# Kernel tuning notes

Measured on AMD Instinct MI355X. Metric: run time of the kernel, lower is better.

Reference implementation:

```python
import jax, jax.numpy as jnp
import numpy as np

N_HEAD = 16
HEAD_DIM = 64


def setup_inputs() -> dict:
    key = jax.random.key(0)
    k1, k2, k3 = jax.random.split(key, 3)
    B, T, C = 1, 4096, 1024
    x = jax.random.normal(k1, (B, T, C), dtype=jnp.float32)
    w_attn = jax.random.normal(k2, (3 * C, C), dtype=jnp.float32) * (C ** -0.5)
    w_proj = jax.random.normal(k3, (C, C), dtype=jnp.float32) * (C ** -0.5)
    return {"x": x, "w_attn": w_attn, "w_proj": w_proj}


def reference(x, w_attn, w_proj):
    B, T, C = x.shape
    H, D = N_HEAD, HEAD_DIM
    qkv = jnp.einsum('btc,fc->btf', x, w_attn)  # [B,T,3C]
    q, k, v = jnp.split(qkv, 3, axis=-1)
    # [B,H,T,D]
    q = q.reshape(B, T, H, D).transpose(0, 2, 1, 3)
    k = k.reshape(B, T, H, D).transpose(0, 2, 1, 3)
    v = v.reshape(B, T, H, D).transpose(0, 2, 1, 3)
    scale = 1.0 / (D ** 0.5)
    att = jnp.einsum('bhqd,bhkd->bhqk', q, k) * scale  # [B,H,T,T]
    causal = jnp.tril(jnp.ones((T, T), dtype=bool))
    att = jnp.where(causal[None, None], att, -jnp.inf)
    att = jax.nn.softmax(att, axis=-1)
    y = jnp.einsum('bhqk,bhkd->bhqd', att, v)  # [B,H,T,D]
    y = y.transpose(0, 2, 1, 3).reshape(B, T, C)
    return jnp.einsum('btc,oc->bto', y, w_proj)
```

## Files before the change

### kernel.cpp

```cpp
#include <hip/hip_runtime.h>

typedef unsigned short u16;
typedef __bf16 bf16x8 __attribute__((ext_vector_type(8)));
typedef float f32x4 __attribute__((ext_vector_type(4)));

__device__ __forceinline__ u16 f2bf(float f) {
  union { float f; unsigned u; } v; v.f = f;
  return (u16)((v.u + 0x7fffu + ((v.u >> 16) & 1u)) >> 16);
}
__device__ __forceinline__ float bf2f(u16 h) {
  union { unsigned u; float f; } v; v.u = ((unsigned)h) << 16;
  return v.f;
}

__device__ __forceinline__ unsigned pkbf(float lo, float hi) {
  union { float f; unsigned u; } a, b; a.f = lo; b.f = hi;
  return __builtin_amdgcn_perm(b.u + 0x8000u, a.u + 0x8000u, 0x07060302u);
}

__device__ __forceinline__ float fexp2(float x) {
#if __has_builtin(__builtin_amdgcn_exp2f)
  return __builtin_amdgcn_exp2f(x);
#else
  return exp2f(x);
#endif
}

__device__ __forceinline__ void gld16(const u16* g, u16* l) {
  __builtin_amdgcn_global_load_lds(
      (const __attribute__((address_space(1))) void*)g,
      (__attribute__((address_space(3))) void*)l, 16, 0, 0);
}


__global__ __launch_bounds__(256) void cvt3(
    const float* __restrict__ x, const float* __restrict__ wa,
    const float* __restrict__ wp, u16* __restrict__ xb,
    u16* __restrict__ wab, u16* __restrict__ wpb)
{
  int b = blockIdx.x;
  const float* in; u16* out; int i;
  if (b < 2048)      { in = x;  out = xb;  i = b * 256 + threadIdx.x; }
  else if (b < 3584) { in = wa; out = wab; i = (b - 2048) * 256 + threadIdx.x; }
  else               { in = wp; out = wpb; i = (b - 3584) * 256 + threadIdx.x; }
  const float* p = in + (size_t)i * 8;
  float4 a = *(const float4*)p, c = *(const float4*)(p + 4);
  uint4 o;
  o.x = pkbf(a.x, a.y); o.y = pkbf(a.z, a.w);
  o.z = pkbf(c.x, c.y); o.w = pkbf(c.z, c.w);
  *(uint4*)&out[(size_t)i * 8] = o;
}

__global__ __launch_bounds__(256) void combine2(
    const u16* __restrict__ O0, const u16* __restrict__ O1,
    const float* __restrict__ l0, const float* __restrict__ l1,
    u16* __restrict__ y)
{
  int i = blockIdx.x * 256 + threadIdx.x;
  int e0 = i * 8;
  int row = e0 >> 10, h = (e0 & 1023) >> 6;
  float inv = 1.0f / (l0[row * 16 + h] + l1[row * 16 + h]);
  uint4 a = *(const uint4*)&O0[(size_t)e0];
  uint4 b = *(const uint4*)&O1[(size_t)e0];
  unsigned aw[4] = {a.x, a.y, a.z, a.w}, bw[4] = {b.x, b.y, b.z, b.w};
  uint4 o;
  unsigned ow[4];
#pragma unroll
  for (int j = 0; j < 4; ++j) {
    float lo = (bf2f((u16)(aw[j] & 0xffffu)) + bf2f((u16)(bw[j] & 0xffffu))) * inv;
    float hi = (bf2f((u16)(aw[j] >> 16))     + bf2f((u16)(bw[j] >> 16)))     * inv;
    ow[j] = pkbf(lo, hi);
  }
  o.x = ow[0]; o.y = ow[1]; o.z = ow[2]; o.w = ow[3];
  *(uint4*)&y[(size_t)e0] = o;
}

template<bool COUT_F32, bool VSPLIT>
__global__ __launch_bounds__(256, 3) void gemm_lds(
    const u16* __restrict__ A, const u16* __restrict__ B, void* __restrict__ C,
    u16* __restrict__ C2, int M, int N, int K, int ldc)
{
  __shared__ u16 S[9216];
  u16* As = S;
  u16* Bs = S + 4096;
  const int tid  = threadIdx.x;
  const int wave = tid >> 6, lane = tid & 63;
  const int quad = lane >> 4, ln = lane & 15;
  const int m0 = blockIdx.y * 128, n0 = blockIdx.x * 128;
  const int wm = (wave >> 1) * 64, wn = (wave & 1) * 64;

  const int srow = wave * 32 + (lane >> 2);
  const int scol = (lane & 3) * 8;

  f32x4 acc[4][4] = {};

  for (int k0 = 0; k0 < K; k0 += 32) {
    __syncthreads();
    const u16* ga = A + (size_t)(m0 + srow) * K + k0 + scol;
    const u16* gb = B + (size_t)(n0 + srow) * K + k0 + scol;
    gld16(ga,                  As + wave * 1024);
    gld16(ga + (size_t)16 * K, As + wave * 1024 + 512);
    gld16(gb,                  Bs + wave * 1024);
    gld16(gb + (size_t)16 * K, Bs + wave * 1024 + 512);
    __syncthreads();

    bf16x8 af[4], bfr[4];
#pragma unroll
    for (int i = 0; i < 4; ++i) af[i]  = *(const bf16x8*)&As[(wm + i * 16 + ln) * 32 + quad * 8];
#pragma unroll
    for (int j = 0; j < 4; ++j) bfr[j] = *(const bf16x8*)&Bs[(wn + j * 16 + ln) * 32 + quad * 8];
#pragma unroll
    for (int i = 0; i < 4; ++i)
#pragma unroll
      for (int j = 0; j < 4; ++j)
        acc[i][j] = __builtin_amdgcn_mfma_f32_16x16x32_bf16(af[i], bfr[j], acc[i][j], 0, 0, 0);
  }

  if constexpr (VSPLIT) {
    if (n0 >= 2048) {
      u16 (*Cs)[72] = (u16(*)[72])S;
      __syncthreads();
#pragma unroll
      for (int c = 0; c < 2; ++c) {
        if ((wave >> 1) == c) {
#pragma unroll
          for (int i = 0; i < 4; ++i)
#pragma unroll
            for (int j = 0; j < 4; ++j)
#pragma unroll
              for (int r = 0; r < 4; ++r) {
                int pos = (i >> 1) * 32 + quad * 8 + (i & 1) * 4 + r;
                Cs[wn + j * 16 + ln][pos] = f2bf(acc[i][j][r]);
              }
        }
        __syncthreads();
        {
          int nl = tid >> 1, mseg = (tid & 1) * 32;
#pragma unroll
          for (int s2 = 0; s2 < 4; ++s2) {
            uint4 v4 = *(const uint4*)&Cs[nl][mseg + s2 * 8];
            *(uint4*)&C2[(size_t)(n0 - 2048 + nl) * 4096 + m0 + c * 64 + mseg + s2 * 8] = v4;
          }
        }
        __syncthreads();
      }
      return;
    }
  }

#pragma unroll
  for (int i = 0; i < 4; ++i)
#pragma unroll
    for (int j = 0; j < 4; ++j)
#pragma unroll
      for (int r = 0; r < 4; ++r) {
        int m = m0 + wm + i * 16 + quad * 4 + r;
        int n = n0 + wn + j * 16 + ln;
        if constexpr (COUT_F32)
          ((float*)C)[(size_t)m * ldc + n] = acc[i][j][r];
        else
          ((u16*)C)[(size_t)m * ldc + n] = f2bf(acc[i][j][r]);
      }
}

template<bool COUT_F32>
__global__ __launch_bounds__(256, 4) void gemm_mn(
    const u16* __restrict__ A, const u16* __restrict__ B, void* __restrict__ C,
    int M, int N, int K, int ldc)
{
  __shared__ u16 S[12288];
  const int tid  = threadIdx.x;
  const int wave = tid >> 6, lane = tid & 63;
  const int quad = lane >> 4, ln = lane & 15;
  const int m0 = blockIdx.y * 128, n0 = blockIdx.x * 64;
  const int wm = (wave >> 1) * 64, wn = (wave & 1) * 32;

  const int srow  = wave * 32 + (lane >> 2);
  const int srowB = wave * 16 + (lane >> 2);
  const int scol  = (lane & 3) * 8;

  const u16* gaBase = A + (size_t)(m0 + srow) * K + scol;
  const u16* gbBase = B + (size_t)(n0 + srowB) * K + scol;

  f32x4 acc[4][2] = {};

  {
    gld16(gaBase,                  S + wave * 1024);
    gld16(gaBase + (size_t)16 * K, S + wave * 1024 + 512);
    gld16(gbBase,                  S + 8192 + wave * 512);
  }
  __syncthreads();

  const int NT = K >> 5;
  for (int t = 0; t < NT; ++t) {
    const int cur = t & 1;
    if (t + 1 < NT) {
      const int nxt = cur ^ 1;
      int k0 = (t + 1) << 5;
      gld16(gaBase + k0,                  S + nxt * 4096 + wave * 1024);
      gld16(gaBase + (size_t)16 * K + k0, S + nxt * 4096 + wave * 1024 + 512);
      gld16(gbBase + k0,                  S + 8192 + nxt * 2048 + wave * 512);
    }

    const u16* As = S + cur * 4096;
    const u16* Bs = S + 8192 + cur * 2048;
    bf16x8 af[4], bfr[2];
#pragma unroll
    for (int i = 0; i < 4; ++i) af[i]  = *(const bf16x8*)&As[(wm + i * 16 + ln) * 32 + quad * 8];
#pragma unroll
    for (int j = 0; j < 2; ++j) bfr[j] = *(const bf16x8*)&Bs[(wn + j * 16 + ln) * 32 + quad * 8];
#pragma unroll
    for (int i = 0; i < 4; ++i)
#pragma unroll
      for (int j = 0; j < 2; ++j)
        acc[i][j] = __builtin_amdgcn_mfma_f32_16x16x32_bf16(af[i], bfr[j], acc[i][j], 0, 0, 0);

    __syncthreads();
  }

#pragma unroll
  for (int i = 0; i < 4; ++i)
#pragma unroll
    for (int j = 0; j < 2; ++j)
#pragma unroll
      for (int r = 0; r < 4; ++r) {
        int m = m0 + wm + i * 16 + quad * 4 + r;
        int n = n0 + wn + j * 16 + ln;
        if constexpr (COUT_F32)
          ((float*)C)[(size_t)m * ldc + n] = acc[i][j][r];
        else
          ((u16*)C)[(size_t)m * ldc + n] = f2bf(acc[i][j][r]);
      }
}

template<bool F32>
__device__ __forceinline__ void stage8(u16* dst, const void* base, size_t off) {
  if constexpr (F32) {
    const float* p = (const float*)base + off;
    float4 a = *(const float4*)p;
    float4 b = *(const float4*)(p + 4);
    uint4 q;
    q.x = pkbf(a.x, a.y); q.y = pkbf(a.z, a.w);
    q.z = pkbf(b.x, b.y); q.w = pkbf(b.z, b.w);
    *(uint4*)dst = q;
  } else {
    *(uint4*)dst = *(const uint4*)((const u16*)base + off);
  }
}

template<bool AF32, bool BF32, bool COUT_F32, bool VSPLIT>
__global__ __launch_bounds__(256) void gemm_bt(
    const void* __restrict__ A, const void* __restrict__ B, void* __restrict__ C,
    u16* __restrict__ C2, int M, int N, int K, int ldc)
{
  __shared__ u16 As[128][40];
  __shared__ u16 Bs[128][40];
  const int tid  = threadIdx.x;
  const int wave = tid >> 6, lane = tid & 63;
  const int quad = lane >> 4, ln = lane & 15;
  const int m0 = blockIdx.y * 128, n0 = blockIdx.x * 128;
  const int wm = (wave >> 1) * 64, wn = (wave & 1) * 64;

  f32x4 acc[4][4] = {};

  for (int k0 = 0; k0 < K; k0 += 32) {
    __syncthreads();
#pragma unroll
    for (int i = 0; i < 2; ++i) {
      int idx = tid + i * 256;
      int row = idx >> 2, seg = (idx & 3) * 8;
      stage8<AF32>(&As[row][seg], A, (size_t)(m0 + row) * K + k0 + seg);
      stage8<BF32>(&Bs[row][seg], B, (size_t)(n0 + row) * K + k0 + seg);
    }
    __syncthreads();
    bf16x8 af[4], bfr[4];
#pragma unroll
    for (int i = 0; i < 4; ++i) af[i]  = *(const bf16x8*)&As[wm + i * 16 + ln][quad * 8];
#pragma unroll
    for (int j = 0; j < 4; ++j) bfr[j] = *(const bf16x8*)&Bs[wn + j * 16 + ln][quad * 8];
#pragma unroll
    for (int i = 0; i < 4; ++i)
#pragma unroll
      for (int j = 0; j < 4; ++j)
        acc[i][j] = __builtin_amdgcn_mfma_f32_16x16x32_bf16(af[i], bfr[j], acc[i][j], 0, 0, 0);
  }

  if constexpr (VSPLIT) {
    if (n0 >= 2048) {
      __shared__ u16 Cs[128][72];
#pragma unroll
      for (int c = 0; c < 2; ++c) {
        if ((wave >> 1) == c) {
#pragma unroll
          for (int i = 0; i < 4; ++i)
#pragma unroll
            for (int j = 0; j < 4; ++j)
#pragma unroll
              for (int r = 0; r < 4; ++r) {
                int pos = (i >> 1) * 32 + quad * 8 + (i & 1) * 4 + r;
                Cs[wn + j * 16 + ln][pos] = f2bf(acc[i][j][r]);
              }
        }
        __syncthreads();
        {
          int nl = tid >> 1, mseg = (tid & 1) * 32;
#pragma unroll
          for (int s2 = 0; s2 < 4; ++s2) {
            uint4 v4 = *(const uint4*)&Cs[nl][mseg + s2 * 8];
            *(uint4*)&C2[(size_t)(n0 - 2048 + nl) * 4096 + m0 + c * 64 + mseg + s2 * 8] = v4;
          }
        }
        __syncthreads();
      }
      return;
    }
  }

#pragma unroll
  for (int i = 0; i < 4; ++i)
#pragma unroll
    for (int j = 0; j < 4; ++j)
#pragma unroll
      for (int r = 0; r < 4; ++r) {
        int m = m0 + wm + i * 16 + quad * 4 + r;
        int n = n0 + wn + j * 16 + ln;
        if constexpr (COUT_F32)
          ((float*)C)[(size_t)m * ldc + n] = acc[i][j][r];
        else
          ((u16*)C)[(size_t)m * ldc + n] = f2bf(acc[i][j][r]);
      }
}

struct StageRegs { uint4 k0, k1, v0, v1; };

__device__ __forceinline__ StageRegs attn_stage_load(
    const u16* __restrict__ qk, const u16* __restrict__ vT,
    int h, int kbase, int tid) {
  StageRegs s;
  {
    int key = tid >> 2, seg = (tid & 3) * 16;
    const u16* kp = qk + (size_t)(kbase + key) * 2048 + 1024 + h * 64 + seg;
    s.k0 = *(const uint4*)kp;
    s.k1 = *(const uint4*)(kp + 8);
  }
  {
    int kh = tid >> 7, d = (tid >> 1) & 63, sg = (tid & 1) * 16;
    const u16* vp = vT + (size_t)(h * 64 + d) * 4096 + kbase + kh * 32 + sg;
    s.v0 = *(const uint4*)vp;
    s.v1 = *(const uint4*)(vp + 8);
  }
  return s;
}

template<bool SPLIT>
__global__ __launch_bounds__(256, SPLIT ? 3 : 2) void attn_fwd(
    const u16* __restrict__ qk, const u16* __restrict__ vT,
    u16* __restrict__ out0, u16* __restrict__ out1,
    float* __restrict__ l0buf, float* __restrict__ l1buf)
{
  __shared__ __align__(16) u16 Ks[2][8][65][8];
  __shared__ __align__(16) u16 Vt[2][8][65][8];

  const int tid  = threadIdx.x;
  const int wave = tid >> 6, lane = tid & 63;
  const int quad = lane >> 4, ln = lane & 15;
  const int bx = blockIdx.x;
  int qt, h, ktb, kte;
  u16* oout; float* lout;
  if constexpr (SPLIT) {
    qt = 31 - (bx >> 5);
    int half = (bx >> 4) & 1;
    h = bx & 15;
    ktb = half ? (qt + 1) : 0;
    kte = half ? (2 * qt + 1) : qt;
    oout = half ? out1 : out0;
    lout = half ? l1buf : l0buf;
  } else {
    qt = (bx < 256) ? (31 - (bx >> 4)) : ((bx - 256) >> 4);
    h = bx & 15;
    ktb = 0; kte = 2 * qt + 1;
    oout = out0; lout = nullptr;
  }
  const float C1 = 0.18033688f;

  const int sq0[2] = { qt * 128 + wave * 32, qt * 128 + wave * 32 + 16 };

  bf16x8 qa[2][2];
#pragma unroll
  for (int s = 0; s < 2; ++s) {
    const u16* qrow = qk + (size_t)(sq0[s] + ln) * 2048 + h * 64;
    qa[s][0] = *(const bf16x8*)(qrow + quad * 8);
    qa[s][1] = *(const bf16x8*)(qrow + 32 + quad * 8);
  }

  bf16x8 ones;
#pragma unroll
  for (int i = 0; i < 8; ++i) ones[i] = (__bf16)1.0f;

  f32x4 o[2][4] = {};
  f32x4 la[2] = {};

  StageRegs st = attn_stage_load(qk, vT, h, ktb * 64, tid);
  int b = 0;
  for (int kt = ktb; kt <= kte; ++kt, b ^= 1) {
    {
      int key = tid >> 2, seg = (tid & 3) * 16;
      int hf = seg >> 5, q0 = (seg & 31) >> 3;
      *(uint4*)&Ks[b][hf * 4 + q0][key][0]     = st.k0;
      *(uint4*)&Ks[b][hf * 4 + q0 + 1][key][0] = st.k1;
      int vh = tid >> 7, d = (tid >> 1) & 63, sq = (tid & 1) * 2;
      *(uint4*)&Vt[b][vh * 4 + sq][d][0]     = st.v0;
      *(uint4*)&Vt[b][vh * 4 + sq + 1][d][0] = st.v1;
    }
    __syncthreads();
    if (kt < kte) st = attn_stage_load(qk, vT, h, (kt + 1) * 64, tid);

    bool act[2];
#pragma unroll
    for (int s = 0; s < 2; ++s) act[s] = (kt * 64 <= sq0[s] + 15);

#pragma unroll 1
    for (int s2 = 0; s2 < 2; ++s2) {
      bf16x8 kf[2][2], vb[4];
#pragma unroll
      for (int hf = 0; hf < 2; ++hf)
#pragma unroll
        for (int tp = 0; tp < 2; ++tp)
          kf[hf][tp] = *(const bf16x8*)&Ks[b][hf * 4 + quad][(s2 * 2 + tp) * 16 + ln][0];
#pragma unroll
      for (int dt = 0; dt < 4; ++dt)
        vb[dt] = *(const bf16x8*)&Vt[b][s2 * 4 + quad][dt * 16 + ln][0];

#pragma unroll
      for (int s = 0; s < 2; ++s) {
        if (!act[s]) continue;
        f32x4 sv[2];
#pragma unroll
        for (int tp = 0; tp < 2; ++tp) {
          f32x4 z = {0.f, 0.f, 0.f, 0.f};
          z = __builtin_amdgcn_mfma_f32_16x16x32_bf16(kf[0][tp], qa[s][0], z, 0, 0, 0);
          z = __builtin_amdgcn_mfma_f32_16x16x32_bf16(kf[1][tp], qa[s][1], z, 0, 0, 0);
          sv[tp] = z;
        }
        float p[2][4];
        if (kt * 64 + 63 > sq0[s]) {
          const int qr = sq0[s] + ln;
#pragma unroll
          for (int tp = 0; tp < 2; ++tp) {
            int keyb = kt * 64 + (s2 * 2 + tp) * 16 + quad * 4;
#pragma unroll
            for (int r = 0; r < 4; ++r) {
              float arg = (keyb + r > qr) ? -200.0f : fmaf(sv[tp][r], C1, -46.0f);
              p[tp][r] = fexp2(arg);
            }
          }
        } else {
#pragma unroll
          for (int tp = 0; tp < 2; ++tp)
#pragma unroll
            for (int r = 0; r < 4; ++r)
              p[tp][r] = fexp2(fmaf(sv[tp][r], C1, -46.0f));
        }
        bf16x8 pv;
        pv[0] = (__bf16)p[0][0]; pv[1] = (__bf16)p[0][1];
        pv[2] = (__bf16)p[0][2]; pv[3] = (__bf16)p[0][3];
        pv[4] = (__bf16)p[1][0]; pv[5] = (__bf16)p[1][1];
        pv[6] = (__bf16)p[1][2]; pv[7] = (__bf16)p[1][3];
        la[s] = __builtin_amdgcn_mfma_f32_16x16x32_bf16(ones, pv, la[s], 0, 0, 0);
#pragma unroll
        for (int dt = 0; dt < 4; ++dt)
          o[s][dt] = __builtin_amdgcn_mfma_f32_16x16x32_bf16(vb[dt], pv, o[s][dt], 0, 0, 0);
      }
    }
  }

#pragma unroll
  for (int s = 0; s < 2; ++s) {
    int rowg = sq0[s] + ln;
    float l_s = la[s][0];
    if constexpr (SPLIT) {
#pragma unroll
      for (int dt = 0; dt < 4; ++dt) {
        uint2 w;
        w.x = pkbf(o[s][dt][0], o[s][dt][1]);
        w.y = pkbf(o[s][dt][2], o[s][dt][3]);
        *(uint2*)&oout[(size_t)rowg * 1024 + h * 64 + dt * 16 + quad * 4] = w;
      }
      if (quad == 0) lout[rowg * 16 + h] = l_s;
    } else {
      float inv = 1.0f / l_s;
#pragma unroll
      for (int dt = 0; dt < 4; ++dt) {
        uint2 w;
        w.x = pkbf(o[s][dt][0] * inv, o[s][dt][1] * inv);
        w.y = pkbf(o[s][dt][2] * inv, o[s][dt][3] * inv);
        *(uint2*)&oout[(size_t)rowg * 1024 + h * 64 + dt * 16 + quad * 4] = w;
      }
    }
  }
}

extern "C" void kernel_launch(void* const* d_in, const int* in_sizes, int n_in,
                              void* d_out, int out_size, void* d_ws, size_t ws_size,
                              hipStream_t stream) {
  const float* x      = (const float*)d_in[0];
  const float* w_attn = (const float*)d_in[1];
  const float* w_proj = (const float*)d_in[2];

  char* ws = (char*)d_ws;
  u16* qk = (u16*)ws;
  u16* vT = (u16*)(ws + (16u << 20));

  if (ws_size >= (size_t)(44u << 20)) {
    u16*   wpb = (u16*)(ws + (24u << 20));
    u16*   xb  = (u16*)(ws + (26u << 20));
    u16*   wab = (u16*)(ws + (34u << 20));
    u16*   Op0 = (u16*)(ws + (26u << 20));
    u16*   Op1 = (u16*)(ws + (34u << 20));
    float* l0  = (float*)(ws + (42u << 20));
    float* l1  = (float*)(ws + (42u << 20) + (256u << 10));
    u16*   y   = (u16*)ws;

    cvt3<<<4096, 256, 0, stream>>>(x, w_attn, w_proj, xb, wab, wpb);
    gemm_lds<false, true><<<dim3(24, 32), 256, 0, stream>>>(
        xb, wab, qk, vT, 4096, 3072, 1024, 2048);
    attn_fwd<true><<<dim3(1024), 256, 0, stream>>>(qk, vT, Op0, Op1, l0, l1);
    combine2<<<2048, 256, 0, stream>>>(Op0, Op1, l0, l1, y);
    gemm_mn<true><<<dim3(16, 32), 256, 0, stream>>>(
        y, wpb, d_out, 4096, 1024, 1024, 1024);
  } else if (ws_size >= (size_t)(40u << 20)) {
    u16* wpb = (u16*)(ws + (24u << 20));
    u16* xb  = (u16*)(ws + (26u << 20));
    u16* wab = (u16*)(ws + (34u << 20));
    u16* y   = (u16*)(ws + (26u << 20));

    cvt3<<<4096, 256, 0, stream>>>(x, w_attn, w_proj, xb, wab, wpb);
    gemm_lds<false, true><<<dim3(24, 32), 256, 0, stream>>>(
        xb, wab, qk, vT, 4096, 3072, 1024, 2048);
    attn_fwd<false><<<dim3(512), 256, 0, stream>>>(qk, vT, y, nullptr, nullptr, nullptr);
    gemm_mn<true><<<dim3(16, 32), 256, 0, stream>>>(
        y, wpb, d_out, 4096, 1024, 1024, 1024);
  } else {
    u16* y = (u16*)(ws + (24u << 20));
    gemm_bt<true, true, false, true><<<dim3(24, 32), 256, 0, stream>>>(
        x, w_attn, qk, vT, 4096, 3072, 1024, 2048);
    attn_fwd<false><<<dim3(512), 256, 0, stream>>>(qk, vT, y, nullptr, nullptr, nullptr);
    gemm_bt<false, true, true, false><<<dim3(8, 32), 256, 0, stream>>>(
        y, w_proj, d_out, nullptr, 4096, 1024, 1024, 1024);
  }
}
```

Measured before the change: 181.5 us.

## Fuse split-K attention combine into attn kernel via atomic ticket handoff

Removes the separate combine2 kernel. The first-finishing half of each split (q-tile, head) pair writes its unnormalized partial O and l and then sets a ready flag. The second half spins on that flag, adds the partial to its own, normalizes, and writes y directly. Flags are zeroed by the cvt3 kernel. This saves one launch and a round trip of O0/O1 through global memory. In exchange it relies on inter-block spin-waiting, which could deadlock if the paired blocks are not co-resident, and it reads the other half's partial through global memory with fences.

```diff
diff --git a/kernel.cpp b/kernel.cpp
--- a/kernel.cpp
+++ b/kernel.cpp
@@ -36,9 +36,13 @@
 __global__ __launch_bounds__(256) void cvt3(
     const float* __restrict__ x, const float* __restrict__ wa,
     const float* __restrict__ wp, u16* __restrict__ xb,
-    u16* __restrict__ wab, u16* __restrict__ wpb)
+    u16* __restrict__ wab, u16* __restrict__ wpb, int* __restrict__ z)
 {
   int b = blockIdx.x;
+  if (z && b == 0) {
+#pragma unroll
+    for (int j = 0; j < 4; ++j) z[threadIdx.x * 4 + j] = 0;
+  }
   const float* in; u16* out; int i;
   if (b < 2048)      { in = x;  out = xb;  i = b * 256 + threadIdx.x; }
   else if (b < 3584) { in = wa; out = wab; i = (b - 2048) * 256 + threadIdx.x; }
@@ -49,30 +53,6 @@
   o.x = pkbf(a.x, a.y); o.y = pkbf(a.z, a.w);
   o.z = pkbf(c.x, c.y); o.w = pkbf(c.z, c.w);
   *(uint4*)&out[(size_t)i * 8] = o;
-}
-
-__global__ __launch_bounds__(256) void combine2(
-    const u16* __restrict__ O0, const u16* __restrict__ O1,
-    const float* __restrict__ l0, const float* __restrict__ l1,
-    u16* __restrict__ y)
-{
-  int i = blockIdx.x * 256 + threadIdx.x;
-  int e0 = i * 8;
-  int row = e0 >> 10, h = (e0 & 1023) >> 6;
-  float inv = 1.0f / (l0[row * 16 + h] + l1[row * 16 + h]);
-  uint4 a = *(const uint4*)&O0[(size_t)e0];
-  uint4 b = *(const uint4*)&O1[(size_t)e0];
-  unsigned aw[4] = {a.x, a.y, a.z, a.w}, bw[4] = {b.x, b.y, b.z, b.w};
-  uint4 o;
-  unsigned ow[4];
-#pragma unroll
-  for (int j = 0; j < 4; ++j) {
-    float lo = (bf2f((u16)(aw[j] & 0xffffu)) + bf2f((u16)(bw[j] & 0xffffu))) * inv;
-    float hi = (bf2f((u16)(aw[j] >> 16))     + bf2f((u16)(bw[j] >> 16)))     * inv;
-    ow[j] = pkbf(lo, hi);
-  }
-  o.x = ow[0]; o.y = ow[1]; o.z = ow[2]; o.w = ow[3];
-  *(uint4*)&y[(size_t)e0] = o;
 }
 
 template<bool COUT_F32, bool VSPLIT>
@@ -355,31 +335,28 @@
 template<bool SPLIT>
 __global__ __launch_bounds__(256, SPLIT ? 3 : 2) void attn_fwd(
     const u16* __restrict__ qk, const u16* __restrict__ vT,
-    u16* __restrict__ out0, u16* __restrict__ out1,
-    float* __restrict__ l0buf, float* __restrict__ l1buf)
+    u16* __restrict__ Op, u16* __restrict__ yout,
+    float* __restrict__ lbuf, int* __restrict__ flagp, int* __restrict__ readyp)
 {
   __shared__ __align__(16) u16 Ks[2][8][65][8];
   __shared__ __align__(16) u16 Vt[2][8][65][8];
+  __shared__ int tkt;
 
   const int tid  = threadIdx.x;
   const int wave = tid >> 6, lane = tid & 63;
   const int quad = lane >> 4, ln = lane & 15;
   const int bx = blockIdx.x;
   int qt, h, ktb, kte;
-  u16* oout; float* lout;
   if constexpr (SPLIT) {
     qt = 31 - (bx >> 5);
     int half = (bx >> 4) & 1;
     h = bx & 15;
     ktb = half ? (qt + 1) : 0;
     kte = half ? (2 * qt + 1) : qt;
-    oout = half ? out1 : out0;
-    lout = half ? l1buf : l0buf;
   } else {
     qt = (bx < 256) ? (31 - (bx >> 4)) : ((bx - 256) >> 4);
     h = bx & 15;
     ktb = 0; kte = 2 * qt + 1;
-    oout = out0; lout = nullptr;
   }
   const float C1 = 0.18033688f;
 
@@ -474,27 +451,61 @@
     }
   }
 
-#pragma unroll
-  for (int s = 0; s < 2; ++s) {
-    int rowg = sq0[s] + ln;
-    float l_s = la[s][0];
-    if constexpr (SPLIT) {
-#pragma unroll
-      for (int dt = 0; dt < 4; ++dt) {
-        uint2 w;
-        w.x = pkbf(o[s][dt][0], o[s][dt][1]);
-        w.y = pkbf(o[s][dt][2], o[s][dt][3]);
-        *(uint2*)&oout[(size_t)rowg * 1024 + h * 64 + dt * 16 + quad * 4] = w;
-      }
-      if (quad == 0) lout[rowg * 16 + h] = l_s;
+  if constexpr (SPLIT) {
+    const int pid = qt * 16 + h;
+    __syncthreads();
+    if (tid == 0) tkt = atomicAdd(flagp + pid, 1);
+    __syncthreads();
+    const int t = tkt;
+    if (t == 0) {
+#pragma unroll
+      for (int s = 0; s < 2; ++s) {
+        int rowg = sq0[s] + ln;
+#pragma unroll
+        for (int dt = 0; dt < 4; ++dt) {
+          uint2 w;
+          w.x = pkbf(o[s][dt][0], o[s][dt][1]);
+          w.y = pkbf(o[s][dt][2], o[s][dt][3]);
+          *(uint2*)&Op[(size_t)rowg * 1024 + h * 64 + dt * 16 + quad * 4] = w;
+        }
+        if (quad == 0) lbuf[rowg * 16 + h] = la[s][0];
+      }
+      __threadfence();
+      __syncthreads();
+      if (tid == 0) atomicExch(readyp + pid, 1);
     } else {
-      float inv = 1.0f / l_s;
+      if (tid == 0) {
+        while (atomicCAS(readyp + pid, 1, 1) == 0) { __builtin_amdgcn_s_sleep(2); }
+      }
+      __syncthreads();
+      __threadfence();
+#pragma unroll
+      for (int s = 0; s < 2; ++s) {
+        int rowg = sq0[s] + ln;
+        float inv = 1.0f / (la[s][0] + lbuf[rowg * 16 + h]);
+#pragma unroll
+        for (int dt = 0; dt < 4; ++dt) {
+          uint2 pw = *(const uint2*)&Op[(size_t)rowg * 1024 + h * 64 + dt * 16 + quad * 4];
+          float v0 = (o[s][dt][0] + bf2f((u16)(pw.x & 0xffffu))) * inv;
+          float v1 = (o[s][dt][1] + bf2f((u16)(pw.x >> 16)))     * inv;
+          float v2 = (o[s][dt][2] + bf2f((u16)(pw.y & 0xffffu))) * inv;
+          float v3 = (o[s][dt][3] + bf2f((u16)(pw.y >> 16)))     * inv;
+          uint2 w; w.x = pkbf(v0, v1); w.y = pkbf(v2, v3);
+          *(uint2*)&yout[(size_t)rowg * 1024 + h * 64 + dt * 16 + quad * 4] = w;
+        }
+      }
+    }
+  } else {
+#pragma unroll
+    for (int s = 0; s < 2; ++s) {
+      int rowg = sq0[s] + ln;
+      float inv = 1.0f / la[s][0];
 #pragma unroll
       for (int dt = 0; dt < 4; ++dt) {
         uint2 w;
         w.x = pkbf(o[s][dt][0] * inv, o[s][dt][1] * inv);
         w.y = pkbf(o[s][dt][2] * inv, o[s][dt][3] * inv);
-        *(uint2*)&oout[(size_t)rowg * 1024 + h * 64 + dt * 16 + quad * 4] = w;
+        *(uint2*)&Op[(size_t)rowg * 1024 + h * 64 + dt * 16 + quad * 4] = w;
       }
     }
   }
@@ -512,20 +523,18 @@
   u16* vT = (u16*)(ws + (16u << 20));
 
   if (ws_size >= (size_t)(44u << 20)) {
-    u16*   wpb = (u16*)(ws + (24u << 20));
-    u16*   xb  = (u16*)(ws + (26u << 20));
-    u16*   wab = (u16*)(ws + (34u << 20));
-    u16*   Op0 = (u16*)(ws + (26u << 20));
-    u16*   Op1 = (u16*)(ws + (34u << 20));
-    float* l0  = (float*)(ws + (42u << 20));
-    float* l1  = (float*)(ws + (42u << 20) + (256u << 10));
-    u16*   y   = (u16*)ws;
-
-    cvt3<<<4096, 256, 0, stream>>>(x, w_attn, w_proj, xb, wab, wpb);
+    u16*   wpb  = (u16*)(ws + (24u << 20));
+    u16*   xb   = (u16*)(ws + (26u << 20));
+    u16*   wab  = (u16*)(ws + (34u << 20));
+    u16*   Op   = (u16*)(ws + (26u << 20));
+    u16*   y    = (u16*)(ws + (34u << 20));
+    float* lbuf = (float*)(ws + (42u << 20));
+    int*   flg  = (int*)(ws + (42u << 20) + (256u << 10));
+
+    cvt3<<<4096, 256, 0, stream>>>(x, w_attn, w_proj, xb, wab, wpb, flg);
     gemm_lds<false, true><<<dim3(24, 32), 256, 0, stream>>>(
         xb, wab, qk, vT, 4096, 3072, 1024, 2048);
-    attn_fwd<true><<<dim3(1024), 256, 0, stream>>>(qk, vT, Op0, Op1, l0, l1);
-    combine2<<<2048, 256, 0, stream>>>(Op0, Op1, l0, l1, y);
+    attn_fwd<true><<<dim3(1024), 256, 0, stream>>>(qk, vT, Op, y, lbuf, flg, flg + 512);
     gemm_mn<true><<<dim3(16, 32), 256, 0, stream>>>(
         y, wpb, d_out, 4096, 1024, 1024, 1024);
   } else if (ws_size >= (size_t)(40u << 20)) {
@@ -534,17 +543,19 @@
     u16* wab = (u16*)(ws + (34u << 20));
     u16* y   = (u16*)(ws + (26u << 20));
 
-    cvt3<<<4096, 256, 0, stream>>>(x, w_attn, w_proj, xb, wab, wpb);
+    cvt3<<<4096, 256, 0, stream>>>(x, w_attn, w_proj, xb, wab, wpb, nullptr);
     gemm_lds<false, true><<<dim3(24, 32), 256, 0, stream>>>(
         xb, wab, qk, vT, 4096, 3072, 1024, 2048);
-    attn_fwd<false><<<dim3(512), 256, 0, stream>>>(qk, vT, y, nullptr, nullptr, nullptr);
+    attn_fwd<false><<<dim3(512), 256, 0, stream>>>(
+        qk, vT, y, nullptr, nullptr, nullptr, nullptr);
     gemm_mn<true><<<dim3(16, 32), 256, 0, stream>>>(
         y, wpb, d_out, 4096, 1024, 1024, 1024);
   } else {
     u16* y = (u16*)(ws + (24u << 20));
     gemm_bt<true, true, false, true><<<dim3(24, 32), 256, 0, stream>>>(
         x, w_attn, qk, vT, 4096, 3072, 1024, 2048);
-    attn_fwd<false><<<dim3(512), 256, 0, stream>>>(qk, vT, y, nullptr, nullptr, nullptr);
+    attn_fwd<false><<<dim3(512), 256, 0, stream>>>(
+        qk, vT, y, nullptr, nullptr, nullptr, nullptr);
     gemm_bt<false, true, true, false><<<dim3(8, 32), 256, 0, stream>>>(
         y, w_proj, d_out, nullptr, 4096, 1024, 1024, 1024);
   }
```

After: 324.2 us. 1.79x slower.
